# Optimization experiments

Hardware: AMD Instinct MI355X
Metric: run time of the kernel (lower is better)

The kernel has to match this reference:

```python
import jax, jax.numpy as jnp
import numpy as np
from functools import partial

L, H, D, T_MAX = 12, 12, 768, 256
HD = D // H
FULL = 302  # 100+100+30+72
LN_EPS = 1e-5


def _ln(x, g, b):
    m = jnp.mean(x, axis=-1, keepdims=True)
    v = jnp.mean((x - m) ** 2, axis=-1, keepdims=True)
    return (x - m) * jax.lax.rsqrt(v + LN_EPS) * g + b


def setup_inputs() -> dict:
    key = jax.random.key(0)
    ks = iter(jax.random.split(key, 40))
    B, T = 64, 256
    w = lambda *s: jax.random.normal(next(ks), s, dtype=jnp.float32) * 0.02
    inp = {
        'idxs': jax.random.randint(next(ks), (B, T, 4), 0, 30, dtype=jnp.int32),
        'lat_emb': w(100, 192), 'lon_emb': w(100, 192),
        'sog_emb': w(30, 192), 'cog_emb': w(72, 192),
        'pos_emb': jnp.zeros((1, T_MAX, D), jnp.float32),
        'ln1_g': jnp.ones((L, D)), 'ln1_b': jnp.zeros((L, D)),
        'ln2_g': jnp.ones((L, D)), 'ln2_b': jnp.zeros((L, D)),
        'Wq': w(L, D, D), 'bq': jnp.zeros((L, D)),
        'Wk': w(L, D, D), 'bk': jnp.zeros((L, D)),
        'Wv': w(L, D, D), 'bv': jnp.zeros((L, D)),
        'Wo': w(L, D, D), 'bo': jnp.zeros((L, D)),
        'W1': w(L, D, 4 * D), 'b1': jnp.zeros((L, 4 * D)),
        'W2': w(L, 4 * D, D), 'b2': jnp.zeros((L, D)),
        'lnf_g': jnp.ones((D,)), 'lnf_b': jnp.zeros((D,)),
        'Whead': w(D, FULL),
    }
    return inp


def _transformer(idxs, lat_emb, lon_emb, sog_emb, cog_emb, pos_emb,
                 ln1_g, ln1_b, ln2_g, ln2_b, Wq, bq, Wk, bk, Wv, bv, Wo, bo,
                 W1, b1, W2, b2, lnf_g, lnf_b, Whead):
    B, T, _ = idxs.shape
    # four-hot embedding: concat of the four attribute embeddings -> [B,T,768]
    h = jnp.concatenate([
        lat_emb[idxs[..., 0]], lon_emb[idxs[..., 1]],
        sog_emb[idxs[..., 2]], cog_emb[idxs[..., 3]],
    ], axis=-1) + pos_emb[:, :T]
    causal = jnp.tril(jnp.ones((T, T), dtype=bool))  # [T,T]
    scale = 1.0 / np.sqrt(HD)

    def block(h, p):
        (g1, b1_, g2, b2_, wq, bq_, wk, bk_, wv, bv_, wo, bo_,
         w1, bf1, w2, bf2) = p
        x = _ln(h, g1, b1_)
        q = (x @ wq + bq_).reshape(B, T, H, HD)
        k = (x @ wk + bk_).reshape(B, T, H, HD)
        v = (x @ wv + bv_).reshape(B, T, H, HD)
        att = jnp.einsum('bqhd,bkhd->bhqk', q, k) * scale
        att = jnp.where(causal, att, -jnp.inf)
        att = jax.nn.softmax(att, axis=-1)
        y = jnp.einsum('bhqk,bkhd->bqhd', att, v).reshape(B, T, D)
        h = h + y @ wo + bo_
        x = _ln(h, g2, b2_)
        h = h + jax.nn.gelu(x @ w1 + bf1, approximate=False) @ w2 + bf2
        return h, None

    stacked = (ln1_g, ln1_b, ln2_g, ln2_b, Wq, bq, Wk, bk, Wv, bv, Wo, bo,
               W1, b1, W2, b2)
    h, _ = jax.lax.scan(block, h, stacked)
    h = _ln(h, lnf_g, lnf_b)
    return h @ Whead  # [B,T,302] logits


def reference(idxs, lat_emb, lon_emb, sog_emb, cog_emb, pos_emb,
              ln1_g, ln1_b, ln2_g, ln2_b, Wq, bq, Wk, bk, Wv, bv, Wo, bo,
              W1, b1, W2, b2, lnf_g, lnf_b, Whead):
    return _transformer(idxs, lat_emb, lon_emb, sog_emb, cog_emb, pos_emb,
                        ln1_g, ln1_b, ln2_g, ln2_b, Wq, bq, Wk, bk, Wv, bv,
                        Wo, bo, W1, b1, W2, b2, lnf_g, lnf_b, Whead)
```

## Files before the change

### kernel.cpp

```cpp
#include <hip/hip_runtime.h>
#include <math.h>


#define LNUM 12
#define HNUM 12
#define DDIM 768
#define HDIM 64
#define TSEQ 256
#define NTOK 16384
#define DFF  3072
#define QKS  1536
#define NOUTC 302
#define NOUTP 384

typedef unsigned short u16;
typedef __attribute__((ext_vector_type(8))) __bf16 bf16x8;
typedef __attribute__((ext_vector_type(8))) unsigned short u16x8;
typedef __attribute__((ext_vector_type(4))) float f32x4;

__device__ __forceinline__ u16 f2bf(float f) {
    union { float f; unsigned u; } v; v.f = f;
    return (u16)((v.u + 0x7fff + ((v.u >> 16) & 1)) >> 16);
}

__device__ __forceinline__ void gl2lds16(const u16* g, u16* l) {
    __builtin_amdgcn_global_load_lds(
        (const __attribute__((address_space(1))) void*)g,
        (__attribute__((address_space(3))) void*)l, 16, 0, 0);
}

__global__ __launch_bounds__(256)
void embed_kernel(const int* __restrict__ idxs, const float* __restrict__ lat,
                  const float* __restrict__ lon, const float* __restrict__ sog,
                  const float* __restrict__ cog, const float* __restrict__ pos,
                  float* __restrict__ h) {
    int i = blockIdx.x * 256 + threadIdx.x;
    int tok = i / DDIM, d = i - tok * DDIM;
    int t = tok & (TSEQ - 1);
    int tab = d / 192, sub = d - tab * 192;
    const float* tp = (tab == 0) ? lat : (tab == 1) ? lon : (tab == 2) ? sog : cog;
    int row = idxs[tok * 4 + tab];
    h[i] = tp[row * 192 + sub] + pos[t * DDIM + d];
}

__global__ __launch_bounds__(256)
void ln_kernel(const float* __restrict__ in, u16* __restrict__ out,
               const float* __restrict__ g, const float* __restrict__ b) {
    const int row = blockIdx.x, t = threadIdx.x;
    const float* x = in + (size_t)row * DDIM;
    float v0 = x[t], v1 = x[t + 256], v2 = x[t + 512];
    float s = v0 + v1 + v2;
    float sq = v0 * v0 + v1 * v1 + v2 * v2;
    #pragma unroll
    for (int m = 32; m; m >>= 1) { s += __shfl_xor(s, m); sq += __shfl_xor(sq, m); }
    __shared__ float red[8];
    const int w = t >> 6;
    if ((t & 63) == 0) { red[w] = s; red[4 + w] = sq; }
    __syncthreads();
    s  = red[0] + red[1] + red[2] + red[3];
    sq = red[4] + red[5] + red[6] + red[7];
    const float mean = s * (1.f / DDIM);
    const float rstd = rsqrtf(sq * (1.f / DDIM) - mean * mean + 1e-5f);
    u16* o = out + (size_t)row * DDIM;
    o[t]       = f2bf((v0 - mean) * rstd * g[t]       + b[t]);
    o[t + 256] = f2bf((v1 - mean) * rstd * g[t + 256] + b[t + 256]);
    o[t + 512] = f2bf((v2 - mean) * rstd * g[t + 512] + b[t + 512]);
}

__global__ __launch_bounds__(256)
void wconv_kernel(const float* __restrict__ in, u16* __restrict__ out,
                  int R, int C, int Cpad) {
    __shared__ float tile[32][33];
    const float* src = in + (size_t)blockIdx.z * R * C;
    u16* dst = out + (size_t)blockIdx.z * (size_t)Cpad * R;
    const int c0 = blockIdx.x * 32, r0 = blockIdx.y * 32;
    const int tx = threadIdx.x & 31, ty = threadIdx.x >> 5;
    #pragma unroll
    for (int i = 0; i < 4; ++i) {
        int r = r0 + ty + i * 8, c = c0 + tx;
        tile[ty + i * 8][tx] = (c < C) ? src[(size_t)r * C + c] : 0.f;
    }
    __syncthreads();
    #pragma unroll
    for (int i = 0; i < 4; ++i) {
        int oc = c0 + ty + i * 8;
        dst[(size_t)oc * R + r0 + tx] = f2bf(tile[tx][ty + i * 8]);
    }
}

template <int MODE>
__global__ __launch_bounds__(256)
void gemm_bt(const u16* __restrict__ A, const u16* __restrict__ Bt,
             const float* __restrict__ bias, const float* __restrict__ bias2,
             const float* __restrict__ bias3, const float* __restrict__ res,
             void* __restrict__ Cout, int M, int N, int K, int ncut) {
    __shared__ u16 As[128][32] __attribute__((aligned(16)));
    __shared__ u16 Bs[128][32] __attribute__((aligned(16)));
    const int t = threadIdx.x;
    const int w = t >> 6, lane = t & 63;
    const int bm = blockIdx.x * 128, bn = blockIdx.y * 128;
    const int moff = (w >> 1) * 64, noff = (w & 1) * 64;
    const int lrow = t >> 2, lcol = (t & 3) * 8;
    const int fm = lane & 15, fq = lane >> 4;
    const f32x4 zero = {0.f, 0.f, 0.f, 0.f};
    f32x4 acc[4][4];
    #pragma unroll
    for (int a = 0; a < 4; ++a)
        #pragma unroll
        for (int c = 0; c < 4; ++c) acc[a][c] = zero;
    const u16* pA = A + (size_t)(bm + lrow) * K + lcol;
    const u16* pB = Bt + (size_t)(bn + lrow) * K + lcol;
    const size_t rstep = (size_t)64 * K;
    u16* asb0 = &As[(w << 4)][0];
    u16* asb1 = &As[64 + (w << 4)][0];
    u16* bsb0 = &Bs[(w << 4)][0];
    u16* bsb1 = &Bs[64 + (w << 4)][0];
    for (int k0 = 0; k0 < K; k0 += 32) {
        __syncthreads();
        gl2lds16(pA, asb0);
        gl2lds16(pA + rstep, asb1);
        gl2lds16(pB, bsb0);
        gl2lds16(pB + rstep, bsb1);
        pA += 32; pB += 32;
        __syncthreads();
        bf16x8 af[4], bfr[4];
        #pragma unroll
        for (int mt = 0; mt < 4; ++mt)
            af[mt] = __builtin_bit_cast(bf16x8, *(const u16x8*)&As[moff + mt * 16 + fm][fq * 8]);
        #pragma unroll
        for (int nt = 0; nt < 4; ++nt)
            bfr[nt] = __builtin_bit_cast(bf16x8, *(const u16x8*)&Bs[noff + nt * 16 + fm][fq * 8]);
        #pragma unroll
        for (int mt = 0; mt < 4; ++mt)
            #pragma unroll
            for (int nt = 0; nt < 4; ++nt)
                acc[mt][nt] = __builtin_amdgcn_mfma_f32_16x16x32_bf16(af[mt], bfr[nt], acc[mt][nt], 0, 0, 0);
    }
    #pragma unroll
    for (int mt = 0; mt < 4; ++mt) {
        #pragma unroll
        for (int nt = 0; nt < 4; ++nt) {
            const int col = bn + noff + nt * 16 + fm;
            float bv = 0.f;
            if (MODE == 5) {
                bv = (col < 768) ? bias[col] : (col < 1536) ? bias2[col - 768] : bias3[col - 1536];
            } else if (MODE != 3) {
                bv = bias[col];
            }
            #pragma unroll
            for (int i = 0; i < 4; ++i) {
                const int row = bm + moff + mt * 16 + fq * 4 + i;
                float v = acc[mt][nt][i] + bv;
                if (MODE == 0) {
                    ((u16*)Cout)[(size_t)row * N + col] = f2bf(v);
                } else if (MODE == 1) {
                    v = 0.5f * v * (1.f + erff(v * 0.70710678118654752f));
                    ((u16*)Cout)[(size_t)row * N + col] = f2bf(v);
                } else if (MODE == 2) {
                    ((float*)Cout)[(size_t)row * N + col] = v + res[(size_t)row * N + col];
                } else if (MODE == 3) {
                    if (col < ncut) ((float*)Cout)[(size_t)row * ncut + col] = v;
                } else {
                    if (col < 1536) {
                        ((u16*)Cout)[(size_t)row * QKS + col] = f2bf(v);
                    } else {
                        const int c = col - 1536;
                        const int bb = row >> 8, tt = row & 255;
                        const int hh = c >> 6, dd = c & 63;
                        u16* vt = (u16*)Cout + (size_t)NTOK * QKS;
                        vt[(((size_t)(bb * HNUM + hh)) * HDIM + dd) * TSEQ + tt] = f2bf(v);
                    }
                }
            }
        }
    }
}

__global__ __launch_bounds__(256)
void attn_kernel(const u16* __restrict__ QK, const u16* __restrict__ Vt,
                 u16* __restrict__ Yb) {
    __shared__ u16 Pt[4][256][16] __attribute__((aligned(16)));
    const int bh = blockIdx.x;
    const int b = bh / HNUM, hh = bh - b * HNUM;
    const int w = threadIdx.x >> 6, lane = threadIdx.x & 63;
    const int fm = lane & 15, fq = lane >> 4;
    const int qt = blockIdx.y * 4 + w;
    const size_t qrow0 = (size_t)b * TSEQ;
    const int col0 = hh * HDIM;
    const u16* qp = QK + (qrow0 + qt * 16 + fm) * QKS + col0 + fq * 8;
    const bf16x8 aq0 = __builtin_bit_cast(bf16x8, *(const u16x8*)qp);
    const bf16x8 aq1 = __builtin_bit_cast(bf16x8, *(const u16x8*)(qp + 32));
    f32x4 s[16];
    #pragma unroll
    for (int kt = 0; kt < 16; ++kt) {
        if (kt <= qt) {
            const u16* kp = QK + (qrow0 + kt * 16 + fm) * QKS + 768 + col0 + fq * 8;
            bf16x8 bk0 = __builtin_bit_cast(bf16x8, *(const u16x8*)kp);
            bf16x8 bk1 = __builtin_bit_cast(bf16x8, *(const u16x8*)(kp + 32));
            f32x4 z = {0.f, 0.f, 0.f, 0.f};
            z = __builtin_amdgcn_mfma_f32_16x16x32_bf16(aq0, bk0, z, 0, 0, 0);
            z = __builtin_amdgcn_mfma_f32_16x16x32_bf16(aq1, bk1, z, 0, 0, 0);
            s[kt] = z;
        }
    }
    float lrow[4];
    #pragma unroll
    for (int i = 0; i < 4; ++i) {
        float mx = -1e30f;
        #pragma unroll
        for (int kt = 0; kt < 16; ++kt) {
            if (kt <= qt) {
                const bool valid = (kt < qt) || (fm <= fq * 4 + i);
                const float v = valid ? s[kt][i] * 0.125f : -1e30f;
                s[kt][i] = v;
                mx = fmaxf(mx, v);
            }
        }
        #pragma unroll
        for (int d = 1; d < 16; d <<= 1) mx = fmaxf(mx, __shfl_xor(mx, d));
        float sum = 0.f;
        #pragma unroll
        for (int kt = 0; kt < 16; ++kt) {
            if (kt <= qt) {
                const float e = __expf(s[kt][i] - mx);
                s[kt][i] = e;
                sum += e;
            }
        }
        #pragma unroll
        for (int d = 1; d < 16; d <<= 1) sum += __shfl_xor(sum, d);
        lrow[i] = sum;
    }
    const int nks = (qt + 2) >> 1;
    #pragma unroll
    for (int kt = 0; kt < 16; ++kt) {
        if (kt < 2 * nks) {
            unsigned lo = 0, hi = 0;
            if (kt <= qt) {
                lo = (unsigned)f2bf(s[kt][0]) | ((unsigned)f2bf(s[kt][1]) << 16);
                hi = (unsigned)f2bf(s[kt][2]) | ((unsigned)f2bf(s[kt][3]) << 16);
            }
            uint2 pk; pk.x = lo; pk.y = hi;
            *(uint2*)&Pt[w][kt * 16 + fm][fq * 4] = pk;
        }
    }
    __syncthreads();
    f32x4 o[4];
    #pragma unroll
    for (int dt = 0; dt < 4; ++dt) o[dt] = (f32x4){0.f, 0.f, 0.f, 0.f};
    #pragma unroll
    for (int ks = 0; ks < 8; ++ks) {
        if (ks < nks) {
            u16x8 praw;
            #pragma unroll
            for (int j = 0; j < 8; ++j) praw[j] = Pt[w][ks * 32 + fq * 8 + j][fm];
            const bf16x8 pa = __builtin_bit_cast(bf16x8, praw);
            #pragma unroll
            for (int dt = 0; dt < 4; ++dt) {
                const u16* vp = Vt + ((size_t)bh * HDIM + dt * 16 + fm) * TSEQ + ks * 32 + fq * 8;
                const bf16x8 bv = __builtin_bit_cast(bf16x8, *(const u16x8*)vp);
                o[dt] = __builtin_amdgcn_mfma_f32_16x16x32_bf16(pa, bv, o[dt], 0, 0, 0);
            }
        }
    }
    #pragma unroll
    for (int i = 0; i < 4; ++i) {
        const float inv = 1.f / lrow[i];
        #pragma unroll
        for (int dt = 0; dt < 4; ++dt)
            Yb[(qrow0 + qt * 16 + fq * 4 + i) * DDIM + col0 + dt * 16 + fm] = f2bf(o[dt][i] * inv);
    }
}

extern "C" void kernel_launch(void* const* d_in, const int* in_sizes, int n_in,
                              void* d_out, int out_size, void* d_ws, size_t ws_size,
                              hipStream_t stream) {
    (void)in_sizes; (void)n_in; (void)out_size; (void)ws_size;
    const int*   idxs  = (const int*)d_in[0];
    const float* lat   = (const float*)d_in[1];
    const float* lon   = (const float*)d_in[2];
    const float* sog   = (const float*)d_in[3];
    const float* cog   = (const float*)d_in[4];
    const float* pos   = (const float*)d_in[5];
    const float* ln1_g = (const float*)d_in[6];
    const float* ln1_b = (const float*)d_in[7];
    const float* ln2_g = (const float*)d_in[8];
    const float* ln2_b = (const float*)d_in[9];
    const float* Wq = (const float*)d_in[10];
    const float* bq = (const float*)d_in[11];
    const float* Wk = (const float*)d_in[12];
    const float* bk = (const float*)d_in[13];
    const float* Wv = (const float*)d_in[14];
    const float* bv = (const float*)d_in[15];
    const float* Wo = (const float*)d_in[16];
    const float* bo = (const float*)d_in[17];
    const float* W1 = (const float*)d_in[18];
    const float* b1 = (const float*)d_in[19];
    const float* W2 = (const float*)d_in[20];
    const float* b2 = (const float*)d_in[21];
    const float* lnf_g = (const float*)d_in[22];
    const float* lnf_b = (const float*)d_in[23];
    const float* Whead = (const float*)d_in[24];

    char* base = (char*)d_ws;
    size_t off = 0;
    auto carve = [&](size_t bytes) { void* r = base + off; off += (bytes + 255) & ~(size_t)255; return r; };
    float* h  = (float*)carve((size_t)NTOK * DDIM * 4);
    u16* xb = (u16*)carve((size_t)NTOK * DDIM * 2);
    u16* qk = (u16*)carve((size_t)NTOK * QKS * 2);
    u16* vt = (u16*)carve((size_t)NTOK * DDIM * 2);
    u16* yb = (u16*)carve((size_t)NTOK * DDIM * 2);
    u16* ub = qk;
    u16* WtQKV = (u16*)carve((size_t)3 * DDIM * DDIM * 2);
    u16* WtO = (u16*)carve((size_t)DDIM * DDIM * 2);
    u16* Wt1 = (u16*)carve((size_t)DDIM * DFF * 2);
    u16* Wt2 = (u16*)carve((size_t)DFF * DDIM * 2);
    u16* WtH = (u16*)carve((size_t)NOUTP * DDIM * 2);

    embed_kernel<<<NTOK * DDIM / 256, 256, 0, stream>>>(idxs, lat, lon, sog, cog, pos, h);

    const dim3 g768(128, 6), g3072(128, 24), gqkv(128, 18), ghead(128, 3);
    const dim3 tq(24, 24, 1), t1(96, 24, 1), t2(24, 96, 1);
    const size_t wsq = (size_t)DDIM * DDIM, wsf = (size_t)DDIM * DFF;
    for (int l = 0; l < LNUM; ++l) {
        wconv_kernel<<<tq, 256, 0, stream>>>(Wq + l * wsq, WtQKV, DDIM, DDIM, DDIM);
        wconv_kernel<<<tq, 256, 0, stream>>>(Wk + l * wsq, WtQKV + wsq, DDIM, DDIM, DDIM);
        wconv_kernel<<<tq, 256, 0, stream>>>(Wv + l * wsq, WtQKV + 2 * wsq, DDIM, DDIM, DDIM);
        wconv_kernel<<<tq, 256, 0, stream>>>(Wo + l * wsq, WtO, DDIM, DDIM, DDIM);
        wconv_kernel<<<t1, 256, 0, stream>>>(W1 + l * wsf, Wt1, DDIM, DFF, DFF);
        wconv_kernel<<<t2, 256, 0, stream>>>(W2 + l * wsf, Wt2, DFF, DDIM, DDIM);

        ln_kernel<<<NTOK, 256, 0, stream>>>(h, xb, ln1_g + l * DDIM, ln1_b + l * DDIM);
        gemm_bt<5><<<gqkv, 256, 0, stream>>>(xb, WtQKV, bq + l * DDIM, bk + l * DDIM,
                                             bv + l * DDIM, nullptr, qk,
                                             NTOK, 3 * DDIM, DDIM, 0);
        attn_kernel<<<dim3(768, 4), 256, 0, stream>>>(qk, vt, yb);
        gemm_bt<2><<<g768, 256, 0, stream>>>(yb, WtO, bo + l * DDIM, nullptr, nullptr, h, h,
                                             NTOK, DDIM, DDIM, 0);
        ln_kernel<<<NTOK, 256, 0, stream>>>(h, xb, ln2_g + l * DDIM, ln2_b + l * DDIM);
        gemm_bt<1><<<g3072, 256, 0, stream>>>(xb, Wt1, b1 + l * DFF, nullptr, nullptr, nullptr, ub,
                                              NTOK, DFF, DDIM, 0);
        gemm_bt<2><<<g768, 256, 0, stream>>>(ub, Wt2, b2 + l * DDIM, nullptr, nullptr, h, h,
                                             NTOK, DDIM, DFF, 0);
    }
    ln_kernel<<<NTOK, 256, 0, stream>>>(h, xb, lnf_g, lnf_b);
    wconv_kernel<<<dim3(NOUTP / 32, DDIM / 32, 1), 256, 0, stream>>>(Whead, WtH, DDIM, NOUTC, NOUTP);
    gemm_bt<3><<<ghead, 256, 0, stream>>>(xb, WtH, nullptr, nullptr, nullptr, nullptr, d_out,
                                          NTOK, NOUTP, DDIM, NOUTC);
}
```

Baseline: 7.026 ms.

## Triple-buffer GEMM LDS tiles with async global-to-LDS prefetch two stages ahead

The bf16 MFMA GEMM now keeps three LDS buffers per operand and issues global-to-LDS loads two k-tiles ahead. Each step waits only on the oldest outstanding loads with vmcnt counters, instead of a full sync around every tile. This lets memory latency overlap with MFMA compute. It triples LDS use (48KB per block), which may reduce occupancy, and it depends on the hand-set vmcnt values matching how many instructions gl2lds16 emits.

```diff
diff --git a/kernel.cpp b/kernel.cpp
--- a/kernel.cpp
+++ b/kernel.cpp
@@ -94,8 +94,8 @@
              const float* __restrict__ bias, const float* __restrict__ bias2,
              const float* __restrict__ bias3, const float* __restrict__ res,
              void* __restrict__ Cout, int M, int N, int K, int ncut) {
-    __shared__ u16 As[128][32] __attribute__((aligned(16)));
-    __shared__ u16 Bs[128][32] __attribute__((aligned(16)));
+    __shared__ u16 As[3][128][32] __attribute__((aligned(16)));
+    __shared__ u16 Bs[3][128][32] __attribute__((aligned(16)));
     const int t = threadIdx.x;
     const int w = t >> 6, lane = t & 63;
     const int bm = blockIdx.x * 128, bn = blockIdx.y * 128;
@@ -111,30 +111,42 @@
     const u16* pA = A + (size_t)(bm + lrow) * K + lcol;
     const u16* pB = Bt + (size_t)(bn + lrow) * K + lcol;
     const size_t rstep = (size_t)64 * K;
-    u16* asb0 = &As[(w << 4)][0];
-    u16* asb1 = &As[64 + (w << 4)][0];
-    u16* bsb0 = &Bs[(w << 4)][0];
-    u16* bsb1 = &Bs[64 + (w << 4)][0];
-    for (int k0 = 0; k0 < K; k0 += 32) {
-        __syncthreads();
-        gl2lds16(pA, asb0);
-        gl2lds16(pA + rstep, asb1);
-        gl2lds16(pB, bsb0);
-        gl2lds16(pB + rstep, bsb1);
-        pA += 32; pB += 32;
-        __syncthreads();
+    const int wr = w << 4;
+    auto stage = [&](int s, int b) {
+        const u16* ga = pA + s * 32;
+        const u16* gb = pB + s * 32;
+        gl2lds16(ga,         &As[b][wr][0]);
+        gl2lds16(ga + rstep, &As[b][wr + 64][0]);
+        gl2lds16(gb,         &Bs[b][wr][0]);
+        gl2lds16(gb + rstep, &Bs[b][wr + 64][0]);
+    };
+    const int kts = K >> 5;
+    stage(0, 0);
+    stage(1, 1);
+    int bcur = 0, bpre = 2;
+    for (int kt = 0; kt < kts; ++kt) {
+        if (kt + 2 < kts) stage(kt + 2, bpre);
+        const int ahead = kts - 1 - kt;
+        if (ahead >= 2)      asm volatile("s_waitcnt vmcnt(8)" ::: "memory");
+        else if (ahead == 1) asm volatile("s_waitcnt vmcnt(4)" ::: "memory");
+        else                 asm volatile("s_waitcnt vmcnt(0)" ::: "memory");
+        __builtin_amdgcn_s_barrier();
         bf16x8 af[4], bfr[4];
         #pragma unroll
         for (int mt = 0; mt < 4; ++mt)
-            af[mt] = __builtin_bit_cast(bf16x8, *(const u16x8*)&As[moff + mt * 16 + fm][fq * 8]);
+            af[mt] = __builtin_bit_cast(bf16x8, *(const u16x8*)&As[bcur][moff + mt * 16 + fm][fq * 8]);
         #pragma unroll
         for (int nt = 0; nt < 4; ++nt)
-            bfr[nt] = __builtin_bit_cast(bf16x8, *(const u16x8*)&Bs[noff + nt * 16 + fm][fq * 8]);
+            bfr[nt] = __builtin_bit_cast(bf16x8, *(const u16x8*)&Bs[bcur][noff + nt * 16 + fm][fq * 8]);
+        asm volatile("s_waitcnt lgkmcnt(0)" ::: "memory");
+        __builtin_amdgcn_s_barrier();
         #pragma unroll
         for (int mt = 0; mt < 4; ++mt)
             #pragma unroll
             for (int nt = 0; nt < 4; ++nt)
                 acc[mt][nt] = __builtin_amdgcn_mfma_f32_16x16x32_bf16(af[mt], bfr[nt], acc[mt][nt], 0, 0, 0);
+        bcur = (bcur == 2) ? 0 : bcur + 1;
+        bpre = (bpre == 2) ? 0 : bpre + 1;
     }
     #pragma unroll
     for (int mt = 0; mt < 4; ++mt) {
```

Result: faster. 6.656 ms (-5.3%).
